# Kernel optimization log

Measured on AMD Instinct MI355X. Metric: run time of the kernel, lower is better.

The kernel has to match this reference:

```python
import jax, jax.numpy as jnp
import numpy as np

D_MODEL = 1024
N_HEADS = 16
HEAD = D_MODEL // N_HEADS
B, T = 4, 2048


def setup_inputs() -> dict:
    key = jax.random.key(0)
    ks = jax.random.split(key, 8)
    s = 0.02
    return {
        "x_enc": jax.random.normal(ks[0], (B, T, D_MODEL), dtype=jnp.float32),
        "x_dec": jax.random.normal(ks[1], (B, T, D_MODEL), dtype=jnp.float32),
        "mask": jnp.zeros((B, T, T), dtype=jnp.float32),
        "Wq": jax.random.normal(ks[2], (D_MODEL, D_MODEL), dtype=jnp.float32) * s,
        "bq": jnp.zeros((D_MODEL,), dtype=jnp.float32),
        "Wkv": jax.random.normal(ks[3], (D_MODEL, 2 * D_MODEL), dtype=jnp.float32) * s,
        "bkv": jnp.zeros((2 * D_MODEL,), dtype=jnp.float32),
        "Wo": jax.random.normal(ks[4], (D_MODEL, D_MODEL), dtype=jnp.float32) * s,
        "bo": jnp.zeros((D_MODEL,), dtype=jnp.float32),
    }


def reference(x_enc, x_dec, mask, Wq, bq, Wkv, bkv, Wo, bo):
    b, t, c = x_enc.shape
    # projections
    kv = x_enc @ Wkv + bkv                     # [B,T,2C]
    q = x_dec @ Wq + bq                        # [B,T,C]
    # split heads (replicates torch reshape of interleaved kv)
    kv = kv.reshape(b, t, N_HEADS, 2 * HEAD).transpose(0, 2, 1, 3)  # [B,H,T,2hs]
    q = q.reshape(b, t, N_HEADS, HEAD).transpose(0, 2, 1, 3)        # [B,H,T,hs]
    k, v = kv[..., :HEAD], kv[..., HEAD:]
    # attention
    scores = jnp.einsum("bhqd,bhkd->bhqk", q, k) / np.sqrt(HEAD).astype(np.float32)
    scores = scores + mask[:, None, :, :]      # additive mask, broadcast over heads
    attn = jax.nn.softmax(scores, axis=-1)
    res = jnp.einsum("bhqk,bhkd->bhqd", attn, v)   # [B,H,T,hs]
    res = res.transpose(0, 2, 1, 3).reshape(b, t, c)
    return res @ Wo + bo
```

## Files before the change

### kernel.cpp

```cpp
#include <hip/hip_runtime.h>
#include <hip/hip_bf16.h>
#include <math.h>


#define D_MODEL 1024
#define NH      16
#define HEAD    64
#define BATCH   4
#define SEQ     2048
#define QB      128

#define LOG2E   1.44269504088896f

typedef unsigned int   u32;
typedef unsigned short u16;
typedef __attribute__((ext_vector_type(8))) short s16x8;
typedef __attribute__((ext_vector_type(4))) float f32x4;
typedef __attribute__((ext_vector_type(4))) unsigned int u32v4;

__device__ __forceinline__ u16 tobf(float f) {
    u32 u = __builtin_bit_cast(u32, f);
    return (u16)((u + 0x7fffu + ((u >> 16) & 1u)) >> 16);
}
__device__ __forceinline__ float frombf(u16 u) {
    return __builtin_bit_cast(float, (u32)u << 16);
}
__device__ __forceinline__ u32 cvtpk(float a, float b) {
    u32 r;
    asm("v_cvt_pk_bf16_f32 %0, %1, %2" : "=v"(r) : "v"(a), "v"(b));
    return r;
}

__device__ __forceinline__ void gl_lds16(const void* g, void* l) {
    __builtin_amdgcn_global_load_lds(
        (const __attribute__((address_space(1))) u32*)g,
        (__attribute__((address_space(3))) u32*)l, 16, 0, 0);
}

__global__ __launch_bounds__(256) void cast_bf16(
    const float* __restrict__ in, u16* __restrict__ out, int n)
{
    int i = (blockIdx.x * 256 + threadIdx.x) * 4;
    if (i < n) {
        float4 v = *(const float4*)(in + i);
        ushort4 o = make_ushort4(tobf(v.x), tobf(v.y), tobf(v.z), tobf(v.w));
        *(ushort4*)(out + i) = o;
    }
}

__global__ __launch_bounds__(256) void mask_prep(
    const float* __restrict__ mask, u16* __restrict__ mp)
{
    const size_t gt = (size_t)blockIdx.x * 256 + threadIdx.x;
    const int l = (int)(gt & 63);
    const size_t tile = gt >> 6;
    const int kt = (int)(tile & 127);
    const size_t bq = tile >> 7;
    const int qt = (int)(bq & 127);
    const int b  = (int)(bq >> 7);
    const int q15 = l & 15, quad = l >> 4;
    const int q = qt*16 + q15;
    const int k = (kt >> 2)*64 + ((kt >> 1) & 1)*32 + (kt & 1)*4 + quad*8;
    float4 v = *(const float4*)&mask[((size_t)(b*SEQ + q))*SEQ + k];
    ushort4 o = make_ushort4(tobf(v.x * LOG2E), tobf(v.y * LOG2E),
                             tobf(v.z * LOG2E), tobf(v.w * LOG2E));
    *(ushort4*)&mp[tile*256 + (size_t)l*4] = o;
}

__global__ __launch_bounds__(256) void transpose_cast(
    const float* __restrict__ W, u16* __restrict__ WT, int K, int N)
{
    __shared__ __align__(16) float tile[32][33];
    const int n0 = blockIdx.x * 32, k0 = blockIdx.y * 32;
    const int r = threadIdx.x >> 3, c4 = (threadIdx.x & 7) * 4;
    float4 v = *(const float4*)&W[(size_t)(k0 + r) * N + n0 + c4];
    tile[r][c4] = v.x; tile[r][c4+1] = v.y; tile[r][c4+2] = v.z; tile[r][c4+3] = v.w;
    __syncthreads();
    ushort4 o = make_ushort4(tobf(tile[c4+0][r]), tobf(tile[c4+1][r]),
                             tobf(tile[c4+2][r]), tobf(tile[c4+3][r]));
    *(ushort4*)&WT[(size_t)(n0 + r) * K + k0 + c4] = o;
}

__device__ __forceinline__ void store_out(u16* p, float v)  { *p = tobf(v); }
__device__ __forceinline__ void store_out(float* p, float v){ *p = v; }

template <typename OT>
__global__ __launch_bounds__(256) void gemm_bt(
    const u16* __restrict__ A, const u16* __restrict__ Bt,
    const float* __restrict__ bias, OT* __restrict__ C,
    int N, int K, float out_scale)
{
    __shared__ __align__(16) u16 As[128 * 32];
    __shared__ __align__(16) u16 Bs[128 * 32];
    const int t = threadIdx.x;
    const int w = t >> 6, l = t & 63;
    const int lane15 = l & 15, quad = l >> 4;
    const int m0 = blockIdx.y * 128, n0 = blockIdx.x * 128;
    const int wm = (w >> 1) * 64, wn = (w & 1) * 64;
    const int lr = l >> 2, lk = (l & 3) * 8;

    f32x4 acc[4][4] = {};

    for (int k0 = 0; k0 < K; k0 += 32) {
        __syncthreads();
        #pragma unroll
        for (int i = 0; i < 2; ++i) {
            const int chunk = w * 2 + i;
            gl_lds16(A  + (size_t)(m0 + chunk*16 + lr) * K + k0 + lk,
                     As + chunk * 512);
            gl_lds16(Bt + (size_t)(n0 + chunk*16 + lr) * K + k0 + lk,
                     Bs + chunk * 512);
        }
        __syncthreads();
        s16x8 af[4], bfr[4];
        #pragma unroll
        for (int i = 0; i < 4; ++i)
            af[i] = *(const s16x8*)&As[(wm + i*16 + lane15) * 32 + quad * 8];
        #pragma unroll
        for (int j = 0; j < 4; ++j)
            bfr[j] = *(const s16x8*)&Bs[(wn + j*16 + lane15) * 32 + quad * 8];
        #pragma unroll
        for (int i = 0; i < 4; ++i)
            #pragma unroll
            for (int j = 0; j < 4; ++j)
                acc[i][j] = __builtin_amdgcn_mfma_f32_16x16x32_bf16(
                    af[i], bfr[j], acc[i][j], 0, 0, 0);
    }
    #pragma unroll
    for (int j = 0; j < 4; ++j) {
        const int col = n0 + wn + j*16 + lane15;
        const float bv = bias[col];
        #pragma unroll
        for (int i = 0; i < 4; ++i)
            #pragma unroll
            for (int r = 0; r < 4; ++r) {
                const int row = m0 + wm + i*16 + quad*4 + r;
                store_out(C + (size_t)row * N + col, (acc[i][j][r] + bv) * out_scale);
            }
    }
}

__global__ __launch_bounds__(256) void v_transpose(
    const u16* __restrict__ kvb, u16* __restrict__ vt)
{
    __shared__ __align__(16) u16 tile[64][72];
    const int t  = threadIdx.x;
    const int t0 = blockIdx.x * 64;
    const int bh = blockIdx.y;
    const int b = bh >> 4, h = bh & 15;
    const int r = t >> 2, c = (t & 3) * 16;
    const u16* g = kvb + (size_t)(b*SEQ + t0 + r) * (2*D_MODEL) + h*128 + 64 + c;
    *(uint4*)&tile[r][c]     = *(const uint4*)g;
    *(uint4*)&tile[r][c + 8] = *(const uint4*)(g + 8);
    __syncthreads();
    u16 buf[16];
    #pragma unroll
    for (int i = 0; i < 16; ++i) buf[i] = tile[c + i][r];
    u16* o = vt + (size_t)(bh*64 + r) * SEQ + t0 + c;
    *(uint4*)o       = *(uint4*)&buf[0];
    *(uint4*)(o + 8) = *(uint4*)&buf[8];
}

__global__ __launch_bounds__(256, 4) void attn_mfma(
    const u16* __restrict__ qb, const u16* __restrict__ kvb,
    const u16* __restrict__ vt, const u16* __restrict__ mp,
    u16* __restrict__ resb)
{
    __shared__ __align__(16) u16 sm[4*4096];
    const int t = threadIdx.x;
    const int w = t >> 6, l = t & 63;
    const int lane15 = l & 15, quad = l >> 4;
    const int h  = blockIdx.x;
    const int q0 = blockIdx.y * QB;
    const int b  = blockIdx.z;
    const int bh = b * NH + h;
    const int lr4 = l >> 2;
    const int lc8 = (((l & 3) ^ (lr4 & 3)) * 8);
    const int cq  = (quad ^ (lane15 & 3)) * 8;
    const int kprow = (lr4 >> 2)*8 + (lr4 & 3);

    s16x8 aq0[2], aq1[2];
    #pragma unroll
    for (int s = 0; s < 2; ++s) {
        const u16* qrow = qb + (size_t)(b*SEQ + q0 + w*32 + s*16 + lane15) * D_MODEL + h*HEAD;
        aq0[s] = *(const s16x8*)(qrow + quad*8);
        aq1[s] = *(const s16x8*)(qrow + 32 + quad*8);
    }
    const u16* mrow[2];
    #pragma unroll
    for (int s = 0; s < 2; ++s)
        mrow[s] = mp + (((size_t)b*128 + (q0>>4) + w*2 + s) * 128) * 256 + (size_t)l*4;

    auto stage = [&](int k0s, int bf) {
        #pragma unroll
        for (int i = 0; i < 2; ++i) {
            const int c = w*2 + i;
            const int hh = c & 1, rr = c >> 1;
            const int krow = (rr >> 1)*32 + (rr & 1)*4 + kprow;
            const u16* kg = kvb + (size_t)(b*SEQ + k0s + krow) * (2*D_MODEL)
                                + h*128 + hh*32 + lc8;
            gl_lds16(kg, sm + bf*4096 + hh*2048 + rr*512);
            const u16* vg = vt + (size_t)(bh*64 + rr*16 + lr4) * SEQ
                               + k0s + hh*32 + lc8;
            gl_lds16(vg, sm + 8192 + bf*4096 + hh*2048 + rr*512);
        }
    };

    f32x4 o_acc[2][4] = {};
    f32x4 l_acc[2] = {};
    ushort4 mreg[2][4];
    s16x8 vones;
    #pragma unroll
    for (int i = 0; i < 8; ++i) vones[i] = (short)0x3F80;

    stage(0, 0);
    #pragma unroll
    for (int s = 0; s < 2; ++s)
        #pragma unroll
        for (int nt = 0; nt < 4; ++nt)
            mreg[s][nt] = *(const ushort4*)(mrow[s] + (size_t)nt * 256);

    for (int it = 0; it < SEQ/64; ++it) {
        const int k0 = it * 64;
        const int bf = it & 1;
        __syncthreads();
        if (it + 1 < SEQ/64)
            stage(k0 + 64, bf ^ 1);

        f32x4 sv[2][4];
        #pragma unroll
        for (int s = 0; s < 2; ++s)
            #pragma unroll
            for (int nt = 0; nt < 4; ++nt) {
                sv[s][nt][0] = frombf(mreg[s][nt].x); sv[s][nt][1] = frombf(mreg[s][nt].y);
                sv[s][nt][2] = frombf(mreg[s][nt].z); sv[s][nt][3] = frombf(mreg[s][nt].w);
            }
        __builtin_amdgcn_s_setprio(1);
        #pragma unroll
        for (int nt = 0; nt < 4; ++nt) {
            s16x8 kf0 = *(const s16x8*)(sm + bf*4096 +        (nt*16 + lane15)*32 + cq);
            s16x8 kf1 = *(const s16x8*)(sm + bf*4096 + 2048 + (nt*16 + lane15)*32 + cq);
            #pragma unroll
            for (int s = 0; s < 2; ++s) {
                sv[s][nt] = __builtin_amdgcn_mfma_f32_16x16x32_bf16(kf0, aq0[s], sv[s][nt], 0, 0, 0);
                sv[s][nt] = __builtin_amdgcn_mfma_f32_16x16x32_bf16(kf1, aq1[s], sv[s][nt], 0, 0, 0);
            }
        }
        __builtin_amdgcn_s_setprio(0);

        if (it + 1 < SEQ/64) {
            #pragma unroll
            for (int s = 0; s < 2; ++s)
                #pragma unroll
                for (int nt = 0; nt < 4; ++nt)
                    mreg[s][nt] = *(const ushort4*)(mrow[s] + ((size_t)((k0+64)>>4) + nt) * 256);
        }

        s16x8 pf[2][2];
        #pragma unroll
        for (int s = 0; s < 2; ++s)
            #pragma unroll
            for (int hf = 0; hf < 2; ++hf) {
                u32v4 pk;
                pk[0] = cvtpk(exp2f(sv[s][2*hf][0]),   exp2f(sv[s][2*hf][1]));
                pk[1] = cvtpk(exp2f(sv[s][2*hf][2]),   exp2f(sv[s][2*hf][3]));
                pk[2] = cvtpk(exp2f(sv[s][2*hf+1][0]), exp2f(sv[s][2*hf+1][1]));
                pk[3] = cvtpk(exp2f(sv[s][2*hf+1][2]), exp2f(sv[s][2*hf+1][3]));
                pf[s][hf] = __builtin_bit_cast(s16x8, pk);
            }

        __builtin_amdgcn_s_setprio(1);
        #pragma unroll
        for (int s = 0; s < 2; ++s) {
            l_acc[s] = __builtin_amdgcn_mfma_f32_16x16x32_bf16(vones, pf[s][0], l_acc[s], 0, 0, 0);
            l_acc[s] = __builtin_amdgcn_mfma_f32_16x16x32_bf16(vones, pf[s][1], l_acc[s], 0, 0, 0);
        }
        #pragma unroll
        for (int dt = 0; dt < 4; ++dt) {
            s16x8 vf0 = *(const s16x8*)(sm + 8192 + bf*4096 +        (dt*16 + lane15)*32 + cq);
            s16x8 vf1 = *(const s16x8*)(sm + 8192 + bf*4096 + 2048 + (dt*16 + lane15)*32 + cq);
            #pragma unroll
            for (int s = 0; s < 2; ++s) {
                o_acc[s][dt] = __builtin_amdgcn_mfma_f32_16x16x32_bf16(vf0, pf[s][0], o_acc[s][dt], 0, 0, 0);
                o_acc[s][dt] = __builtin_amdgcn_mfma_f32_16x16x32_bf16(vf1, pf[s][1], o_acc[s][dt], 0, 0, 0);
            }
        }
        __builtin_amdgcn_s_setprio(0);
    }

    __syncthreads();
    #pragma unroll
    for (int s = 0; s < 2; ++s) {
        const float inv = 1.f / l_acc[s][0];
        u16* orow = &sm[(w*32 + s*16 + lane15) * 72];
        #pragma unroll
        for (int dt = 0; dt < 4; ++dt) {
            *(uint2*)&orow[dt*16 + quad*4] = make_uint2(
                cvtpk(o_acc[s][dt][0]*inv, o_acc[s][dt][1]*inv),
                cvtpk(o_acc[s][dt][2]*inv, o_acc[s][dt][3]*inv));
        }
    }
    __syncthreads();
    {
        const int tr = t >> 1, tc = (t & 1) * 32;
        u16* o = resb + (size_t)(b*SEQ + q0 + tr) * D_MODEL + h*HEAD + tc;
        #pragma unroll
        for (int j = 0; j < 4; ++j)
            *(uint4*)(o + j*8) = *(const uint4*)&sm[tr*72 + tc + j*8];
    }
}

extern "C" void kernel_launch(void* const* d_in, const int* in_sizes, int n_in,
                              void* d_out, int out_size, void* d_ws, size_t ws_size,
                              hipStream_t stream) {
    const float* x_enc = (const float*)d_in[0];
    const float* x_dec = (const float*)d_in[1];
    const float* mask  = (const float*)d_in[2];
    const float* Wq    = (const float*)d_in[3];
    const float* bq    = (const float*)d_in[4];
    const float* Wkv   = (const float*)d_in[5];
    const float* bkv   = (const float*)d_in[6];
    const float* Wo    = (const float*)d_in[7];
    const float* bo    = (const float*)d_in[8];
    float* out = (float*)d_out;

    const int M = BATCH * SEQ;
    u16* xe   = (u16*)d_ws;
    u16* xd   = xe   + (size_t)M * D_MODEL;
    u16* wqT  = xd   + (size_t)M * D_MODEL;
    u16* wkvT = wqT  + (size_t)D_MODEL * D_MODEL;
    u16* woT  = wkvT + (size_t)2*D_MODEL*D_MODEL;
    u16* qbuf = woT  + (size_t)D_MODEL * D_MODEL;
    u16* kvb  = qbuf + (size_t)M * D_MODEL;
    u16* vtb  = kvb  + (size_t)M * 2 * D_MODEL;
    u16* resb = vtb  + (size_t)BATCH*NH*HEAD*SEQ;
    u16* mpk  = xe;

    const int NX = M * D_MODEL;
    cast_bf16<<<NX/1024, 256, 0, stream>>>(x_enc, xe, NX);
    cast_bf16<<<NX/1024, 256, 0, stream>>>(x_dec, xd, NX);
    transpose_cast<<<dim3(D_MODEL/32, D_MODEL/32), 256, 0, stream>>>(Wq,  wqT,  D_MODEL, D_MODEL);
    transpose_cast<<<dim3(2*D_MODEL/32, D_MODEL/32), 256, 0, stream>>>(Wkv, wkvT, D_MODEL, 2*D_MODEL);
    transpose_cast<<<dim3(D_MODEL/32, D_MODEL/32), 256, 0, stream>>>(Wo,  woT,  D_MODEL, D_MODEL);

    gemm_bt<u16><<<dim3(2*D_MODEL/128, M/128), 256, 0, stream>>>(
        xe, wkvT, bkv, kvb, 2*D_MODEL, D_MODEL, 1.0f);
    gemm_bt<u16><<<dim3(D_MODEL/128, M/128), 256, 0, stream>>>(
        xd, wqT, bq, qbuf, D_MODEL, D_MODEL, 0.125f * LOG2E);
    mask_prep<<<(BATCH*128*128*64)/256, 256, 0, stream>>>(mask, mpk);
    v_transpose<<<dim3(SEQ/64, BATCH*NH), 256, 0, stream>>>(kvb, vtb);
    attn_mfma<<<dim3(NH, SEQ/QB, BATCH), 256, 0, stream>>>(
        qbuf, kvb, vtb, mpk, resb);
    gemm_bt<float><<<dim3(D_MODEL/128, M/128), 256, 0, stream>>>(
        resb, woT, bo, out, D_MODEL, D_MODEL, 1.0f);
}
```

Baseline: 427.7 us.

## Double-buffer GEMM LDS tiles and widen attention blocks to 512 threads

The projection GEMM now uses two LDS buffers, issuing the next K-tile's global-to-LDS load before computing on the current one, with a single barrier per iteration. The attention kernel doubles its query block to 256 rows with 8 waves, so each wave stages one K/V chunk instead of two and the K/V tile is shared across more queries. The output staging stride drops from 72 to 64 so 256 rows fit in the existing shared buffer, which can add LDS bank conflicts. Larger attention blocks halve the grid size and may lower occupancy under the (512,4) launch bound.

```diff
diff --git a/kernel.cpp b/kernel.cpp
--- a/kernel.cpp
+++ b/kernel.cpp
@@ -8,7 +8,7 @@
 #define HEAD    64
 #define BATCH   4
 #define SEQ     2048
-#define QB      128
+#define QB      256
 
 #define LOG2E   1.44269504088896f
 
@@ -90,8 +90,8 @@
     const float* __restrict__ bias, OT* __restrict__ C,
     int N, int K, float out_scale)
 {
-    __shared__ __align__(16) u16 As[128 * 32];
-    __shared__ __align__(16) u16 Bs[128 * 32];
+    __shared__ __align__(16) u16 As[2][128 * 32];
+    __shared__ __align__(16) u16 Bs[2][128 * 32];
     const int t = threadIdx.x;
     const int w = t >> 6, l = t & 63;
     const int lane15 = l & 15, quad = l >> 4;
@@ -99,32 +99,38 @@
     const int wm = (w >> 1) * 64, wn = (w & 1) * 64;
     const int lr = l >> 2, lk = (l & 3) * 8;
 
-    f32x4 acc[4][4] = {};
-
-    for (int k0 = 0; k0 < K; k0 += 32) {
-        __syncthreads();
+    auto stage = [&](int k0, int bufi) {
         #pragma unroll
         for (int i = 0; i < 2; ++i) {
             const int chunk = w * 2 + i;
             gl_lds16(A  + (size_t)(m0 + chunk*16 + lr) * K + k0 + lk,
-                     As + chunk * 512);
+                     &As[bufi][chunk * 512]);
             gl_lds16(Bt + (size_t)(n0 + chunk*16 + lr) * K + k0 + lk,
-                     Bs + chunk * 512);
-        }
+                     &Bs[bufi][chunk * 512]);
+        }
+    };
+
+    f32x4 acc[4][4] = {};
+    const int nb = K >> 5;
+    stage(0, 0);
+
+    for (int i = 0; i < nb; ++i) {
+        const int cur = i & 1;
         __syncthreads();
+        if (i + 1 < nb) stage((i + 1) << 5, cur ^ 1);
         s16x8 af[4], bfr[4];
         #pragma unroll
-        for (int i = 0; i < 4; ++i)
-            af[i] = *(const s16x8*)&As[(wm + i*16 + lane15) * 32 + quad * 8];
+        for (int i2 = 0; i2 < 4; ++i2)
+            af[i2] = *(const s16x8*)&As[cur][(wm + i2*16 + lane15) * 32 + quad * 8];
         #pragma unroll
         for (int j = 0; j < 4; ++j)
-            bfr[j] = *(const s16x8*)&Bs[(wn + j*16 + lane15) * 32 + quad * 8];
-        #pragma unroll
-        for (int i = 0; i < 4; ++i)
+            bfr[j] = *(const s16x8*)&Bs[cur][(wn + j*16 + lane15) * 32 + quad * 8];
+        #pragma unroll
+        for (int i2 = 0; i2 < 4; ++i2)
             #pragma unroll
             for (int j = 0; j < 4; ++j)
-                acc[i][j] = __builtin_amdgcn_mfma_f32_16x16x32_bf16(
-                    af[i], bfr[j], acc[i][j], 0, 0, 0);
+                acc[i2][j] = __builtin_amdgcn_mfma_f32_16x16x32_bf16(
+                    af[i2], bfr[j], acc[i2][j], 0, 0, 0);
     }
     #pragma unroll
     for (int j = 0; j < 4; ++j) {
@@ -161,7 +167,7 @@
     *(uint4*)(o + 8) = *(uint4*)&buf[8];
 }
 
-__global__ __launch_bounds__(256, 4) void attn_mfma(
+__global__ __launch_bounds__(512, 4) void attn_mfma(
     const u16* __restrict__ qb, const u16* __restrict__ kvb,
     const u16* __restrict__ vt, const u16* __restrict__ mp,
     u16* __restrict__ resb)
@@ -192,18 +198,14 @@
         mrow[s] = mp + (((size_t)b*128 + (q0>>4) + w*2 + s) * 128) * 256 + (size_t)l*4;
 
     auto stage = [&](int k0s, int bf) {
-        #pragma unroll
-        for (int i = 0; i < 2; ++i) {
-            const int c = w*2 + i;
-            const int hh = c & 1, rr = c >> 1;
-            const int krow = (rr >> 1)*32 + (rr & 1)*4 + kprow;
-            const u16* kg = kvb + (size_t)(b*SEQ + k0s + krow) * (2*D_MODEL)
-                                + h*128 + hh*32 + lc8;
-            gl_lds16(kg, sm + bf*4096 + hh*2048 + rr*512);
-            const u16* vg = vt + (size_t)(bh*64 + rr*16 + lr4) * SEQ
-                               + k0s + hh*32 + lc8;
-            gl_lds16(vg, sm + 8192 + bf*4096 + hh*2048 + rr*512);
-        }
+        const int hh = w & 1, rr = w >> 1;
+        const int krow = (rr >> 1)*32 + (rr & 1)*4 + kprow;
+        const u16* kg = kvb + (size_t)(b*SEQ + k0s + krow) * (2*D_MODEL)
+                            + h*128 + hh*32 + lc8;
+        gl_lds16(kg, sm + bf*4096 + hh*2048 + rr*512);
+        const u16* vg = vt + (size_t)(bh*64 + rr*16 + lr4) * SEQ
+                           + k0s + hh*32 + lc8;
+        gl_lds16(vg, sm + 8192 + bf*4096 + hh*2048 + rr*512);
     };
 
     f32x4 o_acc[2][4] = {};
@@ -292,7 +294,7 @@
     #pragma unroll
     for (int s = 0; s < 2; ++s) {
         const float inv = 1.f / l_acc[s][0];
-        u16* orow = &sm[(w*32 + s*16 + lane15) * 72];
+        u16* orow = &sm[(w*32 + s*16 + lane15) * 64];
         #pragma unroll
         for (int dt = 0; dt < 4; ++dt) {
             *(uint2*)&orow[dt*16 + quad*4] = make_uint2(
@@ -306,7 +308,7 @@
         u16* o = resb + (size_t)(b*SEQ + q0 + tr) * D_MODEL + h*HEAD + tc;
         #pragma unroll
         for (int j = 0; j < 4; ++j)
-            *(uint4*)(o + j*8) = *(const uint4*)&sm[tr*72 + tc + j*8];
+            *(uint4*)(o + j*8) = *(const uint4*)&sm[tr*64 + tc + j*8];
     }
 }
 
@@ -349,7 +351,7 @@
         xd, wqT, bq, qbuf, D_MODEL, D_MODEL, 0.125f * LOG2E);
     mask_prep<<<(BATCH*128*128*64)/256, 256, 0, stream>>>(mask, mpk);
     v_transpose<<<dim3(SEQ/64, BATCH*NH), 256, 0, stream>>>(kvb, vtb);
-    attn_mfma<<<dim3(NH, SEQ/QB, BATCH), 256, 0, stream>>>(
+    attn_mfma<<<dim3(NH, SEQ/QB, BATCH), 512, 0, stream>>>(
         qbuf, kvb, vtb, mpk, resb);
     gemm_bt<float><<<dim3(D_MODEL/128, M/128), 256, 0, stream>>>(
         resb, woT, bo, out, D_MODEL, D_MODEL, 1.0f);
```

Result: faster. 411.6 us (-3.8%).
